# Kernel optimization log

Measured on AMD Instinct MI355X. Metric: run time of the kernel, lower is better.

## Reference

```python
import jax, jax.numpy as jnp
import numpy as np

N_HEAD = 16

def setup_inputs() -> dict:
    key = jax.random.key(0)
    k1, k2, k3 = jax.random.split(key, 3)
    B, S, D = 4, 2048, 1024
    x = jax.random.normal(k1, (B, S, D), dtype=jnp.float32)
    w_attn = jax.random.normal(k2, (D, 3 * D), dtype=jnp.float32) * 0.02
    b_attn = jnp.zeros((3 * D,), dtype=jnp.float32)
    w_proj = jax.random.normal(k3, (D, D), dtype=jnp.float32) * 0.02
    b_proj = jnp.zeros((D,), dtype=jnp.float32)
    return {"x": x, "w_attn": w_attn, "b_attn": b_attn, "w_proj": w_proj, "b_proj": b_proj}

def reference(x, w_attn, b_attn, w_proj, b_proj):
    B, S, D = x.shape
    H = N_HEAD
    dh = D // H
    # c_attn (fan_in_fan_out Conv1D-style: y = x @ W + b)
    qkv = x @ w_attn + b_attn                      # [B,S,3D]
    q, k, v = jnp.split(qkv, 3, axis=-1)
    q = q.reshape(B, S, H, dh).transpose(0, 2, 1, 3)   # [B,H,S,dh]
    k = k.reshape(B, S, H, dh).transpose(0, 2, 3, 1)   # [B,H,dh,S]  (split_heads k=True)
    v = v.reshape(B, S, H, dh).transpose(0, 2, 1, 3)   # [B,H,S,dh]
    # scores = Q K^T, scaled by sqrt(d_head) since scale=True
    w = jnp.einsum('bhid,bhdj->bhij', q, k) / jnp.sqrt(jnp.asarray(dh, x.dtype))
    # causal mask blending exactly as original: w*b - 1e10*(1-b)
    b = jnp.tril(jnp.ones((S, S), dtype=x.dtype))[None, None]
    w = w * b - 1e10 * (1.0 - b)
    w = jax.nn.softmax(w, axis=-1)
    a = jnp.einsum('bhij,bhjd->bhid', w, v)        # [B,H,S,dh]
    a = a.transpose(0, 2, 1, 3).reshape(B, S, D)   # merge_heads
    out = a @ w_proj + b_proj                      # c_proj
    present = jnp.stack((k.transpose(0, 1, 3, 2), v))  # [2,B,H,S,dh]
    return out, present
```

## Files before the change

### kernel.cpp

```cpp
#include <hip/hip_runtime.h>
#include <stdint.h>

typedef unsigned short u16;
typedef __attribute__((ext_vector_type(8))) __bf16 bf16x8;
typedef __attribute__((ext_vector_type(4))) __bf16 bf16x4v;
typedef __attribute__((ext_vector_type(4))) float f32x4;
typedef __attribute__((ext_vector_type(4))) unsigned short u16x4;
typedef __attribute__((ext_vector_type(8))) unsigned short u16x8;

#define MFMA16(a,b,c) __builtin_amdgcn_mfma_f32_16x16x32_bf16(a,b,c,0,0,0)

static __device__ __forceinline__ float fexp2(float x){
#if __has_builtin(__builtin_amdgcn_exp2f)
  return __builtin_amdgcn_exp2f(x);
#else
  float r; asm("v_exp_f32 %0, %1" : "=v"(r) : "v"(x)); return r;
#endif
}

static __device__ __forceinline__ u16 f2b(float f){
  uint32_t u = __float_as_uint(f);
  u += 0x7fffu + ((u >> 16) & 1u);
  return (u16)(u >> 16);
}

static __device__ __forceinline__ void gload_lds16(const void* g, void* l){
  __builtin_amdgcn_global_load_lds(
      (__attribute__((address_space(1))) void*)(uintptr_t)g,
      (__attribute__((address_space(3))) void*)(uintptr_t)l,
      16, 0, 0);
}

__global__ __launch_bounds__(256) void fused_prep(
    const float* __restrict__ x, const float* __restrict__ w_attn,
    const float* __restrict__ w_proj,
    u16* __restrict__ x_bf, u16* __restrict__ wA_T, u16* __restrict__ wP_T)
{
  const int bid = blockIdx.x;
  const int tid = threadIdx.x;
  if (bid < 2048){
    const int n = 4 * 2048 * 1024;
    const int stride = 2048 * 256 * 4;
    int i = (bid * 256 + tid) * 4;
#pragma unroll
    for (int k = 0; k < 4; ++k, i += stride){
      if (i < n){
        float4 v = *(const float4*)(x + i);
        u16x4 o;
        o.x = f2b(v.x); o.y = f2b(v.y); o.z = f2b(v.z); o.w = f2b(v.w);
        *(u16x4*)(x_bf + i) = o;
      }
    }
    return;
  }
  __shared__ float tile[32][33];
  const float* in;
  u16* out;
  int K, N, nb, kb;
  if (bid < 5120){
    const int idx = bid - 2048;
    in = w_attn; out = wA_T; K = 1024; N = 3072;
    nb = (idx % 96) * 32; kb = (idx / 96) * 32;
  } else {
    const int idx = bid - 5120;
    in = w_proj; out = wP_T; K = 1024; N = 1024;
    nb = (idx % 32) * 32; kb = (idx / 32) * 32;
  }
  const int tx = tid & 31, ty = tid >> 5;
#pragma unroll
  for (int i = 0; i < 32; i += 8)
    tile[ty + i][tx] = in[(size_t)(kb + ty + i) * N + nb + tx];
  __syncthreads();
#pragma unroll
  for (int i = 0; i < 32; i += 8)
    out[(size_t)(nb + ty + i) * K + kb + tx] = f2b(tile[tx][ty + i]);
}

template<int MODE>
__global__ __launch_bounds__(256, 2) void gemm_pipe(
    const u16* __restrict__ A, const u16* __restrict__ Bt,
    const float* __restrict__ bias, float* __restrict__ Cout,
    u16* __restrict__ q_bf, u16* __restrict__ k_bf, u16* __restrict__ vT_bf,
    int N, int K)
{
  extern __shared__ u16 smem[];
  const int nT = K >> 5;
  const int tid = threadIdx.x;
  const int w = tid >> 6, lane = tid & 63;
  const int l15 = lane & 15, lhi = lane >> 4;
  const int wr = w >> 1, wc = w & 1;
  const int mBase = blockIdx.y * 256, nBase = blockIdx.x * 128;

  const int qrow = lane >> 2;
  const int ch = (lane & 3) ^ ((qrow >> 1) & 3);
  const u16* AgB = A  + (size_t)(mBase + qrow) * K + ch * 8;
  const u16* BgB = Bt + (size_t)(nBase + qrow) * K + ch * 8;
  const int ln16 = lane << 4;

  f32x4 acc[8][4];
#pragma unroll
  for (int i = 0; i < 8; ++i)
#pragma unroll
    for (int j = 0; j < 4; ++j) acc[i][j] = f32x4{0.f, 0.f, 0.f, 0.f};

  auto stage = [&](int kt){
    char* buf = (char*)smem + (kt % 3) * 24576;
    const int kb = kt << 5;
#pragma unroll
    for (int i = 0; i < 4; ++i)
      gload_lds16(AgB + (size_t)((w * 4 + i) * 16) * K + kb,
                  buf + (w * 4 + i) * 1024 + ln16);
#pragma unroll
    for (int j = 0; j < 2; ++j)
      gload_lds16(BgB + (size_t)((w * 2 + j) * 16) * K + kb,
                  buf + 16384 + (w * 2 + j) * 1024 + ln16);
  };

  stage(0); stage(1);

  for (int kt = 0; kt < nT; ++kt){
    if (kt == nT - 1) asm volatile("s_waitcnt vmcnt(0)" ::: "memory");
    else              asm volatile("s_waitcnt vmcnt(6)" ::: "memory");
    __builtin_amdgcn_s_barrier();
    if (kt + 2 < nT) stage(kt + 2);
    const char* Ab = (const char*)smem + (kt % 3) * 24576;
    const char* Bb = Ab + 16384;
#define LDT(base, row) (*(const bf16x8*)((base) + ((row) << 6) + ((lhi ^ (((row) >> 1) & 3)) << 4)))
    bf16x8 b0, b1, b2, b3, a0, a1, a2, a3;
    {
      const int br = wc * 64 + l15;
      b0 = LDT(Bb, br); b1 = LDT(Bb, br + 16); b2 = LDT(Bb, br + 32); b3 = LDT(Bb, br + 48);
      const int ar = wr * 128 + l15;
      a0 = LDT(Ab, ar); a1 = LDT(Ab, ar + 16); a2 = LDT(Ab, ar + 32); a3 = LDT(Ab, ar + 48);
    }
    __builtin_amdgcn_s_setprio(1);
    acc[0][0] = MFMA16(a0, b0, acc[0][0]); acc[0][1] = MFMA16(a0, b1, acc[0][1]);
    acc[0][2] = MFMA16(a0, b2, acc[0][2]); acc[0][3] = MFMA16(a0, b3, acc[0][3]);
    acc[1][0] = MFMA16(a1, b0, acc[1][0]); acc[1][1] = MFMA16(a1, b1, acc[1][1]);
    acc[1][2] = MFMA16(a1, b2, acc[1][2]); acc[1][3] = MFMA16(a1, b3, acc[1][3]);
    acc[2][0] = MFMA16(a2, b0, acc[2][0]); acc[2][1] = MFMA16(a2, b1, acc[2][1]);
    acc[2][2] = MFMA16(a2, b2, acc[2][2]); acc[2][3] = MFMA16(a2, b3, acc[2][3]);
    acc[3][0] = MFMA16(a3, b0, acc[3][0]); acc[3][1] = MFMA16(a3, b1, acc[3][1]);
    acc[3][2] = MFMA16(a3, b2, acc[3][2]); acc[3][3] = MFMA16(a3, b3, acc[3][3]);
    __builtin_amdgcn_s_setprio(0);
    {
      const int ar = wr * 128 + 64 + l15;
      a0 = LDT(Ab, ar); a1 = LDT(Ab, ar + 16); a2 = LDT(Ab, ar + 32); a3 = LDT(Ab, ar + 48);
    }
#undef LDT
    __builtin_amdgcn_s_setprio(1);
    acc[4][0] = MFMA16(a0, b0, acc[4][0]); acc[4][1] = MFMA16(a0, b1, acc[4][1]);
    acc[4][2] = MFMA16(a0, b2, acc[4][2]); acc[4][3] = MFMA16(a0, b3, acc[4][3]);
    acc[5][0] = MFMA16(a1, b0, acc[5][0]); acc[5][1] = MFMA16(a1, b1, acc[5][1]);
    acc[5][2] = MFMA16(a1, b2, acc[5][2]); acc[5][3] = MFMA16(a1, b3, acc[5][3]);
    acc[6][0] = MFMA16(a2, b0, acc[6][0]); acc[6][1] = MFMA16(a2, b1, acc[6][1]);
    acc[6][2] = MFMA16(a2, b2, acc[6][2]); acc[6][3] = MFMA16(a2, b3, acc[6][3]);
    acc[7][0] = MFMA16(a3, b0, acc[7][0]); acc[7][1] = MFMA16(a3, b1, acc[7][1]);
    acc[7][2] = MFMA16(a3, b2, acc[7][2]); acc[7][3] = MFMA16(a3, b3, acc[7][3]);
    __builtin_amdgcn_s_setprio(0);
  }

  if (MODE == 0){
#pragma unroll
    for (int ni = 0; ni < 4; ++ni){
      const int col = nBase + wc * 64 + ni * 16 + l15;
      const float bv = bias[col];
#pragma unroll
      for (int mi = 0; mi < 8; ++mi)
#pragma unroll
        for (int r = 0; r < 4; ++r){
          const int row = mBase + wr * 128 + mi * 16 + lhi * 4 + r;
          Cout[(size_t)row * N + col] = acc[mi][ni][r] + bv;
        }
    }
    return;
  }

  const int sec = nBase >> 10;
  const int nn0 = nBase & 1023;
  const int bb_ = mBase >> 11;
  const int s0  = mBase & 2047;

  if (sec == 2){
#pragma unroll
    for (int ni = 0; ni < 4; ++ni){
      const int c = wc * 64 + ni * 16 + l15;
      const int nn = nn0 + c;
      const int h = nn >> 6, d = nn & 63;
      const float bv = bias[nBase + c];
#pragma unroll
      for (int mi = 0; mi < 8; ++mi){
        const int sb = s0 + wr * 128 + mi * 16 + lhi * 4;
        u16x4 pk;
#pragma unroll
        for (int r = 0; r < 4; ++r){
          const float v = acc[mi][ni][r] + bv;
          pk[r] = f2b(v);
          Cout[16777216 + ((size_t)(bb_ * 16 + h) * 2048 + sb + r) * 64 + d] = v;
        }
        *(u16x4*)(vT_bf + ((size_t)(bb_ * 16 + h) * 64 + d) * 2048 + sb) = pk;
      }
    }
    return;
  }

  __syncthreads();
  const float qscl = (sec == 0) ? 0.1803368801111204f : 1.0f;
#pragma unroll
  for (int ni = 0; ni < 4; ++ni){
    const int c = wc * 64 + ni * 16 + l15;
    const float bv = bias[nBase + c];
#pragma unroll
    for (int mi = 0; mi < 8; ++mi)
#pragma unroll
      for (int r = 0; r < 4; ++r){
        const int rl = wr * 128 + mi * 16 + lhi * 4 + r;
        smem[rl * 128 + (c ^ ((rl & 7) << 3))] = f2b((acc[mi][ni][r] + bv) * qscl);
      }
  }
  if (sec == 1){
#pragma unroll
    for (int ni = 0; ni < 4; ++ni){
      const int c = wc * 64 + ni * 16 + l15;
      const int nn = nn0 + c;
      const int h = nn >> 6, d = nn & 63;
      const float bv = bias[nBase + c];
#pragma unroll
      for (int mi = 0; mi < 8; ++mi)
#pragma unroll
        for (int r = 0; r < 4; ++r){
          const int s = s0 + wr * 128 + mi * 16 + lhi * 4 + r;
          Cout[8388608 + ((size_t)(bb_ * 16 + h) * 2048 + s) * 64 + d] = acc[mi][ni][r] + bv;
        }
    }
  }
  __syncthreads();
  {
    const int row = tid;
    u16* base = (sec == 0 ? q_bf : k_bf);
#pragma unroll
    for (int i = 0; i < 16; ++i){
      const int c0 = i * 8;
      const int h = (nn0 >> 6) + (c0 >> 6);
      u16x8 vv = *(const u16x8*)&smem[row * 128 + (c0 ^ ((row & 7) << 3))];
      *(u16x8*)(base + ((size_t)(bb_ * 16 + h) * 2048 + s0 + row) * 64 + (c0 & 63)) = vv;
    }
  }
}

__global__ __launch_bounds__(256) void attn_kern(
    const u16* __restrict__ q_bf, const u16* __restrict__ k_bf,
    const u16* __restrict__ vT_bf, u16* __restrict__ a_bf)
{
  const int S = 2048;
  const int id = (int)blockIdx.x + 32 * (int)blockIdx.y;
  const int xcd = id & 7, j = id >> 3;
  const int bh = xcd + 8 * (j & 7);
  const int qt = 31 - (j >> 3);

  const int tid = threadIdx.x, w = tid >> 6, lane = tid & 63;
  const int l15 = lane & 15, lhi = lane >> 4;
  const u16* qp = q_bf + (size_t)bh * S * 64;
  const char* kbytes = (const char*)(k_bf + (size_t)bh * S * 64);
  const char* vbytes = (const char*)(vT_bf + (size_t)bh * 64 * S);
  const int b = bh >> 4, h = bh & 15;

  __shared__ u16 Kbuf[2][64 * 64];
  __shared__ u16 Vbuf[2][64 * 64];
  __shared__ u16 P_all[4][16 * 64];
  char* Pc = (char*)&P_all[w][0];
  const int swz = (l15 & 7) << 4;

  const int srow = tid >> 3;
  const int sch  = (tid & 7) ^ (srow & 7);

  const int qr0 = qt * 64 + w * 16;
  const int nStage = qt + 1;

  bf16x8 qf0 = *(const bf16x8*)&qp[(qr0 + l15) * 64 + lhi * 8];
  bf16x8 qf1 = *(const bf16x8*)&qp[(qr0 + l15) * 64 + 32 + lhi * 8];

  f32x4 o[4];
#pragma unroll
  for (int df = 0; df < 4; ++df) o[df] = f32x4{0.f,0.f,0.f,0.f};
  float lsum = 0.f;

  int cur = 0;
  gload_lds16(kbytes + (size_t)srow * 128 + sch * 16,        (char*)Kbuf[0] + w * 1024);
  gload_lds16(kbytes + (size_t)(srow + 32) * 128 + sch * 16, (char*)Kbuf[0] + 4096 + w * 1024);
  gload_lds16(vbytes + (size_t)srow * 4096 + sch * 16,        (char*)Vbuf[0] + w * 1024);
  gload_lds16(vbytes + (size_t)(srow + 32) * 4096 + sch * 16, (char*)Vbuf[0] + 4096 + w * 1024);
  __syncthreads();

  for (int it = 0; it < nStage; ++it){
    const int jb = it * 64;
    if (it + 1 < nStage){
      const char* kb2 = kbytes + (size_t)(jb + 64) * 128;
      const char* vb2 = vbytes + (size_t)(jb + 64) * 2;
      char* kd = (char*)Kbuf[cur ^ 1];
      char* vd = (char*)Vbuf[cur ^ 1];
      gload_lds16(kb2 + (size_t)srow * 128 + sch * 16,        kd + w * 1024);
      gload_lds16(kb2 + (size_t)(srow + 32) * 128 + sch * 16, kd + 4096 + w * 1024);
      gload_lds16(vb2 + (size_t)srow * 4096 + sch * 16,        vd + w * 1024);
      gload_lds16(vb2 + (size_t)(srow + 32) * 4096 + sch * 16, vd + 4096 + w * 1024);
    }
    {
      const char* Kc = (const char*)Kbuf[cur];
      const char* Vc = (const char*)Vbuf[cur];
      f32x4 s[4];
      __builtin_amdgcn_s_setprio(1);
#pragma unroll
      for (int nf = 0; nf < 4; ++nf){
        const bf16x8 kf0 = *(const bf16x8*)(Kc + (((nf * 16 + l15) * 128 + 0 * 64 + lhi * 16) ^ swz));
        const bf16x8 kf1 = *(const bf16x8*)(Kc + (((nf * 16 + l15) * 128 + 1 * 64 + lhi * 16) ^ swz));
        f32x4 z = {0.f, 0.f, 0.f, 0.f};
        z = MFMA16(kf0, qf0, z);
        z = MFMA16(kf1, qf1, z);
        s[nf] = z;
      }
      __builtin_amdgcn_s_setprio(0);
      bf16x8 vf[8];
#pragma unroll
      for (int kk = 0; kk < 2; ++kk)
#pragma unroll
        for (int df = 0; df < 4; ++df)
          vf[kk*4+df] = *(const bf16x8*)(Vc + (((df * 16 + l15) * 128 + kk * 64 + lhi * 16) ^ swz));
      if (it == nStage - 1){
        const int q = qr0 + l15;
#pragma unroll
        for (int nf = 0; nf < 4; ++nf)
#pragma unroll
          for (int r = 0; r < 4; ++r){
            const int kv = jb + nf * 16 + lhi * 4 + r;
            if (kv > q) s[nf][r] = -1e10f;
          }
      }
      float p[16];
#pragma unroll
      for (int nf = 0; nf < 4; ++nf)
#pragma unroll
        for (int r = 0; r < 4; ++r) p[nf*4+r] = fexp2(s[nf][r]);
      lsum += (((p[0]+p[1])+(p[2]+p[3])) + ((p[4]+p[5])+(p[6]+p[7])))
            + (((p[8]+p[9])+(p[10]+p[11])) + ((p[12]+p[13])+(p[14]+p[15])));
#pragma unroll
      for (int nf = 0; nf < 4; ++nf){
        bf16x4v pk;
#pragma unroll
        for (int r = 0; r < 4; ++r) pk[r] = (__bf16)p[nf*4+r];
        *(bf16x4v*)(Pc + ((l15 * 128 + nf * 32 + lhi * 8) ^ swz)) = pk;
      }
      __builtin_amdgcn_s_setprio(1);
#pragma unroll
      for (int kk = 0; kk < 2; ++kk){
        const bf16x8 pa = *(const bf16x8*)(Pc + ((l15 * 128 + kk * 64 + lhi * 16) ^ swz));
#pragma unroll
        for (int df = 0; df < 4; ++df)
          o[df] = MFMA16(pa, vf[kk*4+df], o[df]);
      }
      __builtin_amdgcn_s_setprio(0);
    }
    __syncthreads();
    cur ^= 1;
  }

  {
    float rs = lsum;
    rs += __shfl_xor(rs, 16);
    rs += __shfl_xor(rs, 32);
    const float linv = 1.0f / rs;
    float lr[4];
#pragma unroll
    for (int r = 0; r < 4; ++r)
      lr[r] = __shfl(linv, (lane & 48) | (lhi * 4 + r));
#pragma unroll
    for (int r = 0; r < 4; ++r){
      const int qrow = qr0 + lhi * 4 + r;
#pragma unroll
      for (int df = 0; df < 4; ++df)
        a_bf[((size_t)b * 2048 + qrow) * 1024 + h * 64 + df * 16 + l15] = f2b(o[df][r] * lr[r]);
    }
  }
}

extern "C" void kernel_launch(void* const* d_in, const int* in_sizes, int n_in,
                              void* d_out, int out_size, void* d_ws, size_t ws_size,
                              hipStream_t stream)
{
  const float* x      = (const float*)d_in[0];
  const float* w_attn = (const float*)d_in[1];
  const float* b_attn = (const float*)d_in[2];
  const float* w_proj = (const float*)d_in[3];
  const float* b_proj = (const float*)d_in[4];
  float* out = (float*)d_out;
  char* ws = (char*)d_ws;
  const size_t MB = 1u << 20;
  u16* x_bf  = (u16*)(ws + 0);
  u16* wA_T  = (u16*)(ws + 16 * MB);
  u16* wP_T  = (u16*)(ws + 22 * MB);
  u16* q_bf  = (u16*)(ws + 24 * MB);
  u16* k_bf  = (u16*)(ws + 40 * MB);
  u16* vT_bf = (u16*)(ws + 56 * MB);
  u16* a_bf  = x_bf;

  fused_prep<<<dim3(6144), dim3(256), 0, stream>>>(x, w_attn, w_proj, x_bf, wA_T, wP_T);
  gemm_pipe<1><<<dim3(24, 32), dim3(256), 73728, stream>>>(
      x_bf, wA_T, b_attn, out, q_bf, k_bf, vT_bf, 3072, 1024);
  attn_kern<<<dim3(32, 64), dim3(256), 0, stream>>>(q_bf, k_bf, vT_bf, a_bf);
  gemm_pipe<0><<<dim3(8, 32), dim3(256), 73728, stream>>>(
      a_bf, wP_T, b_proj, out, nullptr, nullptr, nullptr, 1024, 1024);
}
```

Baseline: 170.4 us.

## Use 8-wave 512-thread blocks for QKV GEMM with smaller per-wave tiles

Adds a dedicated QKV projection kernel that keeps the 256x128 block tile but splits it across 8 waves (4x2) instead of 4, so each wave holds a 64x64 accumulator instead of 128x64. Loading uses all 512 threads with a 3-stage LDS ring. The aim is fewer registers per wave and more waves to hide latency and LDS traffic. The trade-off is more LDS reads per MFMA, since each wave reloads A/B fragments for a smaller output tile. The output projection keeps the old 4-wave kernel with only the plain epilogue.

```diff
diff --git a/kernel.cpp b/kernel.cpp
--- a/kernel.cpp
+++ b/kernel.cpp
@@ -76,11 +76,145 @@
     out[(size_t)(nb + ty + i) * K + kb + tx] = f2b(tile[tx][ty + i]);
 }
 
-template<int MODE>
-__global__ __launch_bounds__(256, 2) void gemm_pipe(
+__global__ __launch_bounds__(512, 2) void gemm_pipe8(
     const u16* __restrict__ A, const u16* __restrict__ Bt,
     const float* __restrict__ bias, float* __restrict__ Cout,
     u16* __restrict__ q_bf, u16* __restrict__ k_bf, u16* __restrict__ vT_bf,
+    int N, int K)
+{
+  extern __shared__ u16 smem[];
+  const int nT = K >> 5;
+  const int tid = threadIdx.x;
+  const int w = tid >> 6, lane = tid & 63;
+  const int l15 = lane & 15, lhi = lane >> 4;
+  const int wr = w >> 1, wc = w & 1;
+  const int mBase = blockIdx.y * 256, nBase = blockIdx.x * 128;
+
+  const int r0 = tid >> 2;
+  const int ch = (tid & 3) ^ ((r0 >> 1) & 3);
+  const u16* Ag  = A  + (size_t)(mBase + r0) * K + ch * 8;
+  const u16* Ag2 = Ag + (size_t)128 * K;
+  const u16* Bg  = Bt + (size_t)(nBase + r0) * K + ch * 8;
+
+  f32x4 acc[4][4];
+#pragma unroll
+  for (int i = 0; i < 4; ++i)
+#pragma unroll
+    for (int j = 0; j < 4; ++j) acc[i][j] = f32x4{0.f, 0.f, 0.f, 0.f};
+
+  auto stage = [&](int kt){
+    char* buf = (char*)smem + (kt % 3) * 24576;
+    const int kb = kt << 5;
+    gload_lds16(Ag  + kb, buf + tid * 16);
+    gload_lds16(Ag2 + kb, buf + 8192 + tid * 16);
+    gload_lds16(Bg  + kb, buf + 16384 + tid * 16);
+  };
+
+  stage(0); stage(1);
+
+  for (int kt = 0; kt < nT; ++kt){
+    if (kt == nT - 1) asm volatile("s_waitcnt vmcnt(0)" ::: "memory");
+    else              asm volatile("s_waitcnt vmcnt(3)" ::: "memory");
+    __builtin_amdgcn_s_barrier();
+    if (kt + 2 < nT) stage(kt + 2);
+    const char* Ab = (const char*)smem + (kt % 3) * 24576;
+    const char* Bb = Ab + 16384;
+#define LDT(base, row) (*(const bf16x8*)((base) + ((row) << 6) + ((lhi ^ (((row) >> 1) & 3)) << 4)))
+    bf16x8 a0, a1, a2, a3, b0, b1, b2, b3;
+    {
+      const int ar = wr * 64 + l15;
+      a0 = LDT(Ab, ar); a1 = LDT(Ab, ar + 16); a2 = LDT(Ab, ar + 32); a3 = LDT(Ab, ar + 48);
+      const int br = wc * 64 + l15;
+      b0 = LDT(Bb, br); b1 = LDT(Bb, br + 16); b2 = LDT(Bb, br + 32); b3 = LDT(Bb, br + 48);
+    }
+#undef LDT
+    __builtin_amdgcn_s_setprio(1);
+    acc[0][0] = MFMA16(a0, b0, acc[0][0]); acc[0][1] = MFMA16(a0, b1, acc[0][1]);
+    acc[0][2] = MFMA16(a0, b2, acc[0][2]); acc[0][3] = MFMA16(a0, b3, acc[0][3]);
+    acc[1][0] = MFMA16(a1, b0, acc[1][0]); acc[1][1] = MFMA16(a1, b1, acc[1][1]);
+    acc[1][2] = MFMA16(a1, b2, acc[1][2]); acc[1][3] = MFMA16(a1, b3, acc[1][3]);
+    acc[2][0] = MFMA16(a2, b0, acc[2][0]); acc[2][1] = MFMA16(a2, b1, acc[2][1]);
+    acc[2][2] = MFMA16(a2, b2, acc[2][2]); acc[2][3] = MFMA16(a2, b3, acc[2][3]);
+    acc[3][0] = MFMA16(a3, b0, acc[3][0]); acc[3][1] = MFMA16(a3, b1, acc[3][1]);
+    acc[3][2] = MFMA16(a3, b2, acc[3][2]); acc[3][3] = MFMA16(a3, b3, acc[3][3]);
+    __builtin_amdgcn_s_setprio(0);
+  }
+
+  const int sec = nBase >> 10;
+  const int nn0 = nBase & 1023;
+  const int bb_ = mBase >> 11;
+  const int s0  = mBase & 2047;
+
+  if (sec == 2){
+#pragma unroll
+    for (int ni = 0; ni < 4; ++ni){
+      const int c = wc * 64 + ni * 16 + l15;
+      const int nn = nn0 + c;
+      const int h = nn >> 6, d = nn & 63;
+      const float bv = bias[nBase + c];
+#pragma unroll
+      for (int mi = 0; mi < 4; ++mi){
+        const int sb = s0 + wr * 64 + mi * 16 + lhi * 4;
+        u16x4 pk;
+#pragma unroll
+        for (int r = 0; r < 4; ++r){
+          const float v = acc[mi][ni][r] + bv;
+          pk[r] = f2b(v);
+          Cout[16777216 + ((size_t)(bb_ * 16 + h) * 2048 + sb + r) * 64 + d] = v;
+        }
+        *(u16x4*)(vT_bf + ((size_t)(bb_ * 16 + h) * 64 + d) * 2048 + sb) = pk;
+      }
+    }
+    return;
+  }
+
+  __syncthreads();
+  const float qscl = (sec == 0) ? 0.1803368801111204f : 1.0f;
+#pragma unroll
+  for (int ni = 0; ni < 4; ++ni){
+    const int c = wc * 64 + ni * 16 + l15;
+    const float bv = bias[nBase + c];
+#pragma unroll
+    for (int mi = 0; mi < 4; ++mi)
+#pragma unroll
+      for (int r = 0; r < 4; ++r){
+        const int rl = wr * 64 + mi * 16 + lhi * 4 + r;
+        smem[rl * 128 + (c ^ ((rl & 7) << 3))] = f2b((acc[mi][ni][r] + bv) * qscl);
+      }
+  }
+  if (sec == 1){
+#pragma unroll
+    for (int ni = 0; ni < 4; ++ni){
+      const int c = wc * 64 + ni * 16 + l15;
+      const int nn = nn0 + c;
+      const int h = nn >> 6, d = nn & 63;
+      const float bv = bias[nBase + c];
+#pragma unroll
+      for (int mi = 0; mi < 4; ++mi)
+#pragma unroll
+        for (int r = 0; r < 4; ++r){
+          const int s = s0 + wr * 64 + mi * 16 + lhi * 4 + r;
+          Cout[8388608 + ((size_t)(bb_ * 16 + h) * 2048 + s) * 64 + d] = acc[mi][ni][r] + bv;
+        }
+    }
+  }
+  __syncthreads();
+  {
+    const int row = tid >> 1, half = tid & 1;
+    u16* base = (sec == 0 ? q_bf : k_bf);
+#pragma unroll
+    for (int i = 0; i < 8; ++i){
+      const int c0 = half * 64 + i * 8;
+      const int h = (nn0 >> 6) + (c0 >> 6);
+      u16x8 vv = *(const u16x8*)&smem[row * 128 + (c0 ^ ((row & 7) << 3))];
+      *(u16x8*)(base + ((size_t)(bb_ * 16 + h) * 2048 + s0 + row) * 64 + (c0 & 63)) = vv;
+    }
+  }
+}
+
+__global__ __launch_bounds__(256, 2) void gemm_pipe4(
+    const u16* __restrict__ A, const u16* __restrict__ Bt,
+    const float* __restrict__ bias, float* __restrict__ Cout,
     int N, int K)
 {
   extern __shared__ u16 smem[];
@@ -160,91 +294,17 @@
     __builtin_amdgcn_s_setprio(0);
   }
 
-  if (MODE == 0){
-#pragma unroll
-    for (int ni = 0; ni < 4; ++ni){
-      const int col = nBase + wc * 64 + ni * 16 + l15;
-      const float bv = bias[col];
-#pragma unroll
-      for (int mi = 0; mi < 8; ++mi)
-#pragma unroll
-        for (int r = 0; r < 4; ++r){
-          const int row = mBase + wr * 128 + mi * 16 + lhi * 4 + r;
-          Cout[(size_t)row * N + col] = acc[mi][ni][r] + bv;
-        }
-    }
-    return;
-  }
-
-  const int sec = nBase >> 10;
-  const int nn0 = nBase & 1023;
-  const int bb_ = mBase >> 11;
-  const int s0  = mBase & 2047;
-
-  if (sec == 2){
-#pragma unroll
-    for (int ni = 0; ni < 4; ++ni){
-      const int c = wc * 64 + ni * 16 + l15;
-      const int nn = nn0 + c;
-      const int h = nn >> 6, d = nn & 63;
-      const float bv = bias[nBase + c];
-#pragma unroll
-      for (int mi = 0; mi < 8; ++mi){
-        const int sb = s0 + wr * 128 + mi * 16 + lhi * 4;
-        u16x4 pk;
-#pragma unroll
-        for (int r = 0; r < 4; ++r){
-          const float v = acc[mi][ni][r] + bv;
-          pk[r] = f2b(v);
-          Cout[16777216 + ((size_t)(bb_ * 16 + h) * 2048 + sb + r) * 64 + d] = v;
-        }
-        *(u16x4*)(vT_bf + ((size_t)(bb_ * 16 + h) * 64 + d) * 2048 + sb) = pk;
-      }
-    }
-    return;
-  }
-
-  __syncthreads();
-  const float qscl = (sec == 0) ? 0.1803368801111204f : 1.0f;
 #pragma unroll
   for (int ni = 0; ni < 4; ++ni){
-    const int c = wc * 64 + ni * 16 + l15;
-    const float bv = bias[nBase + c];
+    const int col = nBase + wc * 64 + ni * 16 + l15;
+    const float bv = bias[col];
 #pragma unroll
     for (int mi = 0; mi < 8; ++mi)
 #pragma unroll
       for (int r = 0; r < 4; ++r){
-        const int rl = wr * 128 + mi * 16 + lhi * 4 + r;
-        smem[rl * 128 + (c ^ ((rl & 7) << 3))] = f2b((acc[mi][ni][r] + bv) * qscl);
-      }
-  }
-  if (sec == 1){
-#pragma unroll
-    for (int ni = 0; ni < 4; ++ni){
-      const int c = wc * 64 + ni * 16 + l15;
-      const int nn = nn0 + c;
-      const int h = nn >> 6, d = nn & 63;
-      const float bv = bias[nBase + c];
-#pragma unroll
-      for (int mi = 0; mi < 8; ++mi)
-#pragma unroll
-        for (int r = 0; r < 4; ++r){
-          const int s = s0 + wr * 128 + mi * 16 + lhi * 4 + r;
-          Cout[8388608 + ((size_t)(bb_ * 16 + h) * 2048 + s) * 64 + d] = acc[mi][ni][r] + bv;
-        }
-    }
-  }
-  __syncthreads();
-  {
-    const int row = tid;
-    u16* base = (sec == 0 ? q_bf : k_bf);
-#pragma unroll
-    for (int i = 0; i < 16; ++i){
-      const int c0 = i * 8;
-      const int h = (nn0 >> 6) + (c0 >> 6);
-      u16x8 vv = *(const u16x8*)&smem[row * 128 + (c0 ^ ((row & 7) << 3))];
-      *(u16x8*)(base + ((size_t)(bb_ * 16 + h) * 2048 + s0 + row) * 64 + (c0 & 63)) = vv;
-    }
+        const int row = mBase + wr * 128 + mi * 16 + lhi * 4 + r;
+        Cout[(size_t)row * N + col] = acc[mi][ni][r] + bv;
+      }
   }
 }
 
@@ -403,9 +463,9 @@
   u16* a_bf  = x_bf;
 
   fused_prep<<<dim3(6144), dim3(256), 0, stream>>>(x, w_attn, w_proj, x_bf, wA_T, wP_T);
-  gemm_pipe<1><<<dim3(24, 32), dim3(256), 73728, stream>>>(
+  gemm_pipe8<<<dim3(24, 32), dim3(512), 73728, stream>>>(
       x_bf, wA_T, b_attn, out, q_bf, k_bf, vT_bf, 3072, 1024);
   attn_kern<<<dim3(32, 64), dim3(256), 0, stream>>>(q_bf, k_bf, vT_bf, a_bf);
-  gemm_pipe<0><<<dim3(8, 32), dim3(256), 73728, stream>>>(
-      a_bf, wP_T, b_proj, out, nullptr, nullptr, nullptr, 1024, 1024);
-}
+  gemm_pipe4<<<dim3(8, 32), dim3(256), 73728, stream>>>(
+      a_bf, wP_T, b_proj, out, 1024, 1024);
+}
```

Measured after the change: 175.0 us. 1.03x slower.
